# Performance work log

Measured on AMD Instinct MI355X. Metric: run time of the kernel, lower is better.

## Reference

```python
import jax, jax.numpy as jnp
import numpy as np

B, S, DM = 2, 2048, 1024
H, D = 16, 64  # multiheads, head_dim; H*D == DM
NEG = -1e9


def setup_inputs() -> dict:
    key = jax.random.key(0)
    ks = jax.random.split(key, 7)
    xavier = float(np.sqrt(6.0 / (DM + H * D)))
    return {
        "Q": jax.random.normal(ks[0], (B, S, DM), dtype=jnp.float32),
        "K": jax.random.normal(ks[1], (B, S, DM), dtype=jnp.float32),
        "V": jax.random.normal(ks[2], (B, S, DM), dtype=jnp.float32),
        "V_len": jax.random.randint(ks[3], (B,), 0, S),
        "WQ": jax.random.uniform(ks[4], (DM, H * D), dtype=jnp.float32, minval=-xavier, maxval=xavier),
        "WK": jax.random.uniform(ks[5], (DM, H * D), dtype=jnp.float32, minval=-xavier, maxval=xavier),
        "WV": jax.random.uniform(ks[6], (DM, H * D), dtype=jnp.float32, minval=-xavier, maxval=xavier),
    }


def reference(Q, K, V, V_len, WQ, WK, WV):
    b, s, _ = Q.shape
    # project and split heads: [B,S,DM] -> [B,H,S,D]
    q = (Q @ WQ).reshape(b, s, H, D).transpose(0, 2, 1, 3)
    k = (K @ WK).reshape(b, s, H, D).transpose(0, 2, 1, 3)
    v = (V @ WV).reshape(b, s, H, D).transpose(0, 2, 1, 3)
    scores = jnp.einsum("bhqd,bhkd->bhqk", q, k) / jnp.sqrt(jnp.float32(D))
    # key padding mask: valid keys are positions < V_len[b]
    valid = jnp.arange(s)[None, :] < V_len[:, None]          # [B,S]
    scores = jnp.where(valid[:, None, None, :], scores, NEG)  # [B,H,Sq,Sk]
    attn = jax.nn.softmax(scores, axis=-1)
    out = jnp.einsum("bhqk,bhkd->bhqd", attn, v)
    return out.transpose(0, 2, 1, 3).reshape(b, s, H * D)
```

## Files before the change

### kernel.cpp

```cpp
#include <hip/hip_runtime.h>
#include <hip/hip_bf16.h>

#define NBATCH 2
#define SEQ 2048
#define DMODEL 1024
#define NHEAD 16
#define HDIM 64
#define ROWS (NBATCH*SEQ)

typedef __attribute__((ext_vector_type(8))) short bf16x8;
typedef __attribute__((ext_vector_type(4))) float f32x4;
typedef __attribute__((ext_vector_type(16))) float f32x16;

#define MFMA16 __builtin_amdgcn_mfma_f32_16x16x32_bf16
#define MFMA32 __builtin_amdgcn_mfma_f32_32x32x16_bf16

#define QSCALE 0.1803368801111204f
#define DEFER_THR 11.541560327111708f

static __device__ __forceinline__ unsigned short f2bf(float f) {
    unsigned int u = __float_as_uint(f);
    u += 0x7fffu + ((u >> 16) & 1u);
    return (unsigned short)(u >> 16);
}

static __device__ __forceinline__ unsigned cvtpk(float lo, float hi) {
    unsigned r;
    asm("v_cvt_pk_bf16_f32 %0, %1, %2" : "=v"(r) : "v"(lo), "v"(hi));
    return r;
}

static __device__ __forceinline__ void gld16(const unsigned short* g, unsigned short* l) {
    __builtin_amdgcn_global_load_lds(
        (const __attribute__((address_space(1))) unsigned int*)g,
        (__attribute__((address_space(3))) unsigned int*)l,
        16, 0, 0);
}

__global__ __launch_bounds__(256) void cvt_kernel(const float* __restrict__ Q, const float* __restrict__ K,
                                                  const float* __restrict__ V, const int* __restrict__ vlenp,
                                                  unsigned short* __restrict__ dq, unsigned short* __restrict__ dk,
                                                  unsigned short* __restrict__ dv, int n8) {
    int i = blockIdx.x * 256 + threadIdx.x;
    if (i >= n8) return;
    const int z = blockIdx.z;
    if (z) {
        int row = i >> 7;
        int bb = row >> 11, s = row & 2047;
        int vl = vlenp[bb];
        int lim = ((vl + 31) >> 5) << 5;
        if (z == 1) { if (vl == 0 || s >= lim) return; }
        else        { if (vl != 0 && s >= lim) return; }
    }
    const float* src = z == 0 ? Q : (z == 1 ? K : V);
    unsigned short* dst = z == 0 ? dq : (z == 1 ? dk : dv);
    const float4* s4 = (const float4*)src;
    float4 a = s4[2 * i], b = s4[2 * i + 1];
    union { bf16x8 v; unsigned short u[8]; } o;
    o.u[0] = f2bf(a.x); o.u[1] = f2bf(a.y); o.u[2] = f2bf(a.z); o.u[3] = f2bf(a.w);
    o.u[4] = f2bf(b.x); o.u[5] = f2bf(b.y); o.u[6] = f2bf(b.z); o.u[7] = f2bf(b.w);
    *(bf16x8*)(dst + (size_t)i * 8) = o.v;
}

__global__ __launch_bounds__(256) void wtrans_kernel(const float* __restrict__ W0, const float* __restrict__ W1,
                                                     const float* __restrict__ W2,
                                                     unsigned short* __restrict__ T0, unsigned short* __restrict__ T1,
                                                     unsigned short* __restrict__ T2) {
    const float* W = blockIdx.z == 0 ? W0 : (blockIdx.z == 1 ? W1 : W2);
    unsigned short* T = blockIdx.z == 0 ? T0 : (blockIdx.z == 1 ? T1 : T2);
    __shared__ float tile[64][65];
    int rb = blockIdx.y * 64, cb = blockIdx.x * 64;
    int tid = threadIdx.x;
    #pragma unroll
    for (int rep = 0; rep < 16; ++rep) {
        int idx = rep * 256 + tid; int r = idx >> 6, c = idx & 63;
        tile[r][c] = W[(size_t)(rb + r) * DMODEL + cb + c];
    }
    __syncthreads();
    #pragma unroll
    for (int rep = 0; rep < 16; ++rep) {
        int idx = rep * 256 + tid; int r = idx >> 6, c = idx & 63;
        T[(size_t)(cb + r) * DMODEL + rb + c] = f2bf(tile[c][r]);
    }
}

__global__ __launch_bounds__(256) void proj_kernel(
        const unsigned short* __restrict__ Xq, const unsigned short* __restrict__ Xk,
        const unsigned short* __restrict__ Xv,
        const unsigned short* __restrict__ WTq, const unsigned short* __restrict__ WTk,
        const unsigned short* __restrict__ WTv, const int* __restrict__ vlenp,
        unsigned short* __restrict__ qp, unsigned short* __restrict__ kp,
        unsigned short* __restrict__ vtp) {
    const int mode = blockIdx.z;
    const int rowBase = blockIdx.y * 128;
    const int colBase = blockIdx.x * 128;

    if (mode >= 1) {
        const int bb = rowBase >> 11, sS = rowBase & 2047;
        const int vl = vlenp[bb];
        const int lim = ((vl + 31) >> 5) << 5;
        if (mode == 1) { if (vl == 0 || sS >= lim) return; }
        else           { if (vl != 0 && sS >= lim) return; }
    }

    const unsigned short* X  = mode == 0 ? Xq  : (mode == 1 ? Xk  : Xv);
    const unsigned short* WT = mode == 0 ? WTq : (mode == 1 ? WTk : WTv);

    __shared__ unsigned short As[128 * 64];
    __shared__ unsigned short Bs[128 * 64];

    const int tid = threadIdx.x, lane = tid & 63, w = tid >> 6;
    const int wr = w >> 1, wc = w & 1;

    const int Xwave = (mode < 2) ? wr : wc;
    const int Wwave = (mode < 2) ? wc : wr;

    const int rloc = lane >> 3;
    const int ssw  = ((lane & 7) * 8) ^ (rloc * 8);

    f32x4 acc[4][4];
    #pragma unroll
    for (int i = 0; i < 4; ++i)
        #pragma unroll
        for (int j = 0; j < 4; ++j) acc[i][j] = (f32x4){0.f, 0.f, 0.f, 0.f};

    for (int kt = 0; kt < DMODEL / 64; ++kt) {
        #pragma unroll
        for (int j = 0; j < 4; ++j) {
            int c = w * 4 + j;
            int r = c * 8 + rloc;
            gld16(X  + (size_t)(rowBase + r) * DMODEL + kt * 64 + ssw, &As[c * 512]);
            gld16(WT + (size_t)(colBase + r) * DMODEL + kt * 64 + ssw, &Bs[c * 512]);
        }
        __syncthreads();
        #pragma unroll
        for (int ks = 0; ks < 2; ++ks) {
            const int kbyte = ks * 64 + ((lane >> 4) * 16);
            bf16x8 xf[4], wf[4];
            #pragma unroll
            for (int i = 0; i < 4; ++i) {
                int xr = Xwave * 64 + i * 16 + (lane & 15);
                xf[i] = *(const bf16x8*)((const char*)As + xr * 128 + (kbyte ^ ((xr & 7) << 4)));
                int wrow = Wwave * 64 + i * 16 + (lane & 15);
                wf[i] = *(const bf16x8*)((const char*)Bs + wrow * 128 + (kbyte ^ ((wrow & 7) << 4)));
            }
            if (mode < 2) {
                #pragma unroll
                for (int i = 0; i < 4; ++i)
                    #pragma unroll
                    for (int j = 0; j < 4; ++j)
                        acc[i][j] = MFMA16(xf[i], wf[j], acc[i][j], 0, 0, 0);
            } else {
                #pragma unroll
                for (int i = 0; i < 4; ++i)
                    #pragma unroll
                    for (int j = 0; j < 4; ++j)
                        acc[i][j] = MFMA16(wf[i], xf[j], acc[i][j], 0, 0, 0);
            }
        }
        __syncthreads();
    }

    if (mode < 2) {
        unsigned short* outp = (mode == 0) ? qp : kp;
        const float sc = (mode == 0) ? QSCALE : 1.0f;
        #pragma unroll
        for (int i = 0; i < 4; ++i)
            #pragma unroll
            for (int j = 0; j < 4; ++j)
                #pragma unroll
                for (int r = 0; r < 4; ++r) {
                    int grow = rowBase + wr * 64 + i * 16 + (lane >> 4) * 4 + r;
                    int gcol = colBase + wc * 64 + j * 16 + (lane & 15);
                    int b = grow >> 11, s = grow & 2047, hh = gcol >> 6, d = gcol & 63;
                    outp[((size_t)(b * NHEAD + hh) * SEQ + s) * HDIM + d] = f2bf(acc[i][j][r] * sc);
                }
    } else {
        #pragma unroll
        for (int i = 0; i < 4; ++i)
            #pragma unroll
            for (int j = 0; j < 4; ++j)
                #pragma unroll
                for (int r = 0; r < 4; ++r) {
                    int gcol = colBase + wr * 64 + i * 16 + (lane >> 4) * 4 + r;
                    int grow = rowBase + wc * 64 + j * 16 + (lane & 15);
                    int b = grow >> 11, s = grow & 2047, hh = gcol >> 6, d = gcol & 63;
                    vtp[((size_t)(b * NHEAD + hh) * HDIM + d) * SEQ + s] = f2bf(acc[i][j][r]);
                }
    }
}

__global__ __launch_bounds__(256, 4) void attn_kernel(
        const unsigned short* __restrict__ qp, const unsigned short* __restrict__ kp,
        const unsigned short* __restrict__ vtp, const int* __restrict__ vlenp,
        float* __restrict__ out) {
    const int tid = threadIdx.x, lane = tid & 63, w = tid >> 6;
    const int hh = lane >> 5;
    const int ql = lane & 31;
    const int qsub = w >> 1, kpar = w & 1;
    const int qt = blockIdx.x, h = blockIdx.y, b = blockIdx.z;
    const int vlen = vlenp[b];
    const int nt = (vlen == 0) ? (SEQ / 32) : ((vlen + 31) >> 5);
    const int myn = (nt - kpar + 1) >> 1;

    __shared__ unsigned short Ks[4][2][32 * 64];
    __shared__ float mlb[4][2][32];

    const size_t headQ = (size_t)(b * NHEAD + h) * SEQ * HDIM;
    const size_t headV = (size_t)(b * NHEAD + h) * HDIM * SEQ;

    const int qrow = qt * 64 + qsub * 32 + ql;
    bf16x8 qf[4];
    #pragma unroll
    for (int ks = 0; ks < 4; ++ks)
        qf[ks] = *(const bf16x8*)(qp + headQ + (size_t)qrow * HDIM + ks * 16 + hh * 8);

    f32x16 o0, o1;
    #pragma unroll
    for (int r = 0; r < 16; ++r) { o0[r] = 0.f; o1[r] = 0.f; }
    float m_run = -1e30f, l_run = 0.f;

    const int rloc = lane >> 3;
    const int ssw  = ((lane & 7) * 8) ^ (rloc * 8);

    auto stage = [&](int kvB, int buf) {
        #pragma unroll
        for (int c = 0; c < 4; ++c)
            gld16(kp + headQ + (size_t)(kvB + c * 8 + rloc) * HDIM + ssw, &Ks[w][buf][c * 512]);
    };

    if (myn > 0) stage(kpar * 32, 0);

    for (int i = 0; i < myn; ++i) {
        const int kvBase = (kpar + 2 * i) * 32;
        const int cur = i & 1;
        asm volatile("s_waitcnt vmcnt(0)" ::: "memory");

        bf16x8 vf00 = *(const bf16x8*)(vtp + headV + (size_t)ql * SEQ + kvBase + hh * 8);
        bf16x8 vf01 = *(const bf16x8*)(vtp + headV + (size_t)(32 + ql) * SEQ + kvBase + hh * 8);
        bf16x8 vf10 = *(const bf16x8*)(vtp + headV + (size_t)ql * SEQ + kvBase + 16 + hh * 8);
        bf16x8 vf11 = *(const bf16x8*)(vtp + headV + (size_t)(32 + ql) * SEQ + kvBase + 16 + hh * 8);

        if (i + 1 < myn) stage(kvBase + 64, cur ^ 1);

        const char* Kb = (const char*)&Ks[w][cur][0];
        f32x16 s0;
        #pragma unroll
        for (int r = 0; r < 16; ++r) s0[r] = 0.f;
        __builtin_amdgcn_s_setprio(1);
        #pragma unroll
        for (int ks = 0; ks < 4; ++ks) {
            const int kb = (ks * 32 + hh * 16) ^ ((ql & 7) << 4);
            bf16x8 kf = *(const bf16x8*)(Kb + ql * 128 + kb);
            s0 = MFMA32(kf, qf[ks], s0, 0, 0, 0);
        }
        __builtin_amdgcn_s_setprio(0);

        if (kvBase + 32 > vlen) {
            #pragma unroll
            for (int r = 0; r < 16; ++r) {
                int kl = (r & 3) + 8 * (r >> 2) + 4 * hh;
                if (kvBase + kl >= vlen) s0[r] = -1e9f;
            }
        }

        float mx[8];
        #pragma unroll
        for (int t = 0; t < 8; ++t) mx[t] = fmaxf(s0[t], s0[t + 8]);
        #pragma unroll
        for (int st = 4; st > 0; st >>= 1)
            #pragma unroll
            for (int t = 0; t < st; ++t) mx[t] = fmaxf(mx[t], mx[t + st]);
        float tmax = fmaxf(mx[0], __shfl_xor(mx[0], 32));

        if (!__all(tmax <= m_run + DEFER_THR)) {
            const float mnew = fmaxf(m_run, tmax);
            const float al = __builtin_amdgcn_exp2f(m_run - mnew);
            l_run *= al;
            #pragma unroll
            for (int r = 0; r < 16; ++r) { o0[r] *= al; o1[r] *= al; }
            m_run = mnew;
        }

        #pragma unroll
        for (int r = 0; r < 16; ++r) s0[r] = __builtin_amdgcn_exp2f(s0[r] - m_run);
        float sm[8];
        #pragma unroll
        for (int t = 0; t < 8; ++t) sm[t] = s0[t] + s0[t + 8];
        #pragma unroll
        for (int st = 4; st > 0; st >>= 1)
            #pragma unroll
            for (int t = 0; t < st; ++t) sm[t] += sm[t + st];
        l_run += sm[0] + __shfl_xor(sm[0], 32);

        unsigned d0[8];
        #pragma unroll
        for (int t = 0; t < 8; ++t) d0[t] = cvtpk(s0[2 * t], s0[2 * t + 1]);

        __builtin_amdgcn_s_setprio(1);
#define PV_SLICE(KSL, VFA, VFB)                                                    \
        {                                                                          \
            unsigned a0 = d0[4 * (KSL)],     b0 = d0[4 * (KSL) + 2];               \
            unsigned a1 = d0[4 * (KSL) + 1], b1 = d0[4 * (KSL) + 3];               \
            asm("v_permlane32_swap_b32 %0, %1" : "+v"(a0), "+v"(b0));              \
            asm("v_permlane32_swap_b32 %0, %1" : "+v"(a1), "+v"(b1));              \
            union { unsigned u[4]; bf16x8 v; } pa;                                 \
            pa.u[0] = a0; pa.u[1] = a1; pa.u[2] = b0; pa.u[3] = b1;                \
            o0 = MFMA32(VFA, pa.v, o0, 0, 0, 0);                                   \
            o1 = MFMA32(VFB, pa.v, o1, 0, 0, 0);                                   \
        }
        PV_SLICE(0, vf00, vf01)
        PV_SLICE(1, vf10, vf11)
#undef PV_SLICE
        __builtin_amdgcn_s_setprio(0);
    }

    if (hh == 0) { mlb[w][0][ql] = m_run; mlb[w][1][ql] = l_run; }
    if (kpar == 1) {
        char* Ob = (char*)&Ks[w][0][0];
        #pragma unroll
        for (int g = 0; g < 4; ++g) {
            int ad = ql * 256 + ((32 * g + 16 * hh) ^ (16 * (ql & 7)));
            *(float4*)(Ob + ad)       = make_float4(o0[4*g], o0[4*g+1], o0[4*g+2], o0[4*g+3]);
            *(float4*)(Ob + ad + 128) = make_float4(o1[4*g], o1[4*g+1], o1[4*g+2], o1[4*g+3]);
        }
    }
    __syncthreads();
    if (kpar == 0) {
        const float mp = mlb[w + 1][0][ql], lp = mlb[w + 1][1][ql];
        const float M = fmaxf(m_run, mp);
        const float a0 = __builtin_amdgcn_exp2f(m_run - M);
        const float a1 = __builtin_amdgcn_exp2f(mp - M);
        const float linv = 1.0f / (l_run * a0 + lp * a1);
        const char* Pb = (const char*)&Ks[w + 1][0][0];
        float* orow = out + (size_t)(b * SEQ + qrow) * DMODEL + h * HDIM;
        #pragma unroll
        for (int g = 0; g < 4; ++g) {
            int ad = ql * 256 + ((32 * g + 16 * hh) ^ (16 * (ql & 7)));
            float4 p0 = *(const float4*)(Pb + ad);
            float4 p1 = *(const float4*)(Pb + ad + 128);
            *(float4*)(orow + 8 * g + 4 * hh) = make_float4(
                (o0[4*g]   * a0 + p0.x * a1) * linv, (o0[4*g+1] * a0 + p0.y * a1) * linv,
                (o0[4*g+2] * a0 + p0.z * a1) * linv, (o0[4*g+3] * a0 + p0.w * a1) * linv);
            *(float4*)(orow + 32 + 8 * g + 4 * hh) = make_float4(
                (o1[4*g]   * a0 + p1.x * a1) * linv, (o1[4*g+1] * a0 + p1.y * a1) * linv,
                (o1[4*g+2] * a0 + p1.z * a1) * linv, (o1[4*g+3] * a0 + p1.w * a1) * linv);
        }
    }
}

extern "C" void kernel_launch(void* const* d_in, const int* in_sizes, int n_in,
                              void* d_out, int out_size, void* d_ws, size_t ws_size,
                              hipStream_t stream) {
    const float* Q  = (const float*)d_in[0];
    const float* K  = (const float*)d_in[1];
    const float* V  = (const float*)d_in[2];
    const int* V_len = (const int*)d_in[3];
    const float* WQ = (const float*)d_in[4];
    const float* WK = (const float*)d_in[5];
    const float* WV = (const float*)d_in[6];
    float* out = (float*)d_out;

    char* ws = (char*)d_ws;
    const size_t MB = 1024 * 1024;
    unsigned short* Xq  = (unsigned short*)(ws + 0 * MB);
    unsigned short* Xk  = (unsigned short*)(ws + 8 * MB);
    unsigned short* Xv  = (unsigned short*)(ws + 16 * MB);
    unsigned short* WTq = (unsigned short*)(ws + 24 * MB);
    unsigned short* WTk = (unsigned short*)(ws + 26 * MB);
    unsigned short* WTv = (unsigned short*)(ws + 28 * MB);
    unsigned short* qpj = (unsigned short*)(ws + 30 * MB);
    unsigned short* kpj = (unsigned short*)(ws + 38 * MB);
    unsigned short* vtp = (unsigned short*)(ws + 46 * MB);

    const int n8 = ROWS * DMODEL / 8;
    cvt_kernel<<<dim3((n8 + 255) / 256, 1, 3), 256, 0, stream>>>(Q, K, V, V_len, Xq, Xk, Xv, n8);
    wtrans_kernel<<<dim3(16, 16, 3), 256, 0, stream>>>(WQ, WK, WV, WTq, WTk, WTv);
    proj_kernel<<<dim3(DMODEL / 128, ROWS / 128, 3), 256, 0, stream>>>(
        Xq, Xk, Xv, WTq, WTk, WTv, V_len, qpj, kpj, vtp);
    attn_kernel<<<dim3(SEQ / 64, NHEAD, NBATCH), 256, 0, stream>>>(qpj, kpj, vtp, V_len, out);
}
```

Before: 93.18 us.

## Share K and V tiles in LDS between wave pairs via cooperative staging

The two waves that handle the same key parity but different query sub-tiles now share one K tile and one V tile in LDS instead of each fetching its own. One wave stages the K tile and the other stages the V tile with async global-to-LDS loads, double-buffered. V fragments are read from swizzled LDS rather than loaded per wave straight from global memory. This halves global K/V traffic per block and makes the V reads more coalesced, at the cost of a block-wide __syncthreads each iteration and lockstep progress between waves, plus an extra barrier before the partial-output merge.

```diff
diff --git a/kernel.cpp b/kernel.cpp
--- a/kernel.cpp
+++ b/kernel.cpp
@@ -202,8 +202,10 @@
     const int vlen = vlenp[b];
     const int nt = (vlen == 0) ? (SEQ / 32) : ((vlen + 31) >> 5);
     const int myn = (nt - kpar + 1) >> 1;
-
-    __shared__ unsigned short Ks[4][2][32 * 64];
+    const int J = (nt + 1) >> 1;
+
+    __shared__ unsigned short Kd[2][2][2048];
+    __shared__ unsigned short Vd[2][2][2048];
     __shared__ float mlb[4][2][32];
 
     const size_t headQ = (size_t)(b * NHEAD + h) * SEQ * HDIM;
@@ -222,102 +224,116 @@
 
     const int rloc = lane >> 3;
     const int ssw  = ((lane & 7) * 8) ^ (rloc * 8);
-
-    auto stage = [&](int kvB, int buf) {
+    const int gn   = (lane & 7) ^ rloc;
+    const int koff = (gn & 3) * 8;
+    const int dhi  = (gn >> 2) * 32;
+
+    auto stageK = [&](int kvB, int buf) {
         #pragma unroll
         for (int c = 0; c < 4; ++c)
-            gld16(kp + headQ + (size_t)(kvB + c * 8 + rloc) * HDIM + ssw, &Ks[w][buf][c * 512]);
+            gld16(kp + headQ + (size_t)(kvB + c * 8 + rloc) * HDIM + ssw, &Kd[kpar][buf][c * 512]);
     };
-
-    if (myn > 0) stage(kpar * 32, 0);
-
-    for (int i = 0; i < myn; ++i) {
-        const int kvBase = (kpar + 2 * i) * 32;
-        const int cur = i & 1;
-        asm volatile("s_waitcnt vmcnt(0)" ::: "memory");
-
-        bf16x8 vf00 = *(const bf16x8*)(vtp + headV + (size_t)ql * SEQ + kvBase + hh * 8);
-        bf16x8 vf01 = *(const bf16x8*)(vtp + headV + (size_t)(32 + ql) * SEQ + kvBase + hh * 8);
-        bf16x8 vf10 = *(const bf16x8*)(vtp + headV + (size_t)ql * SEQ + kvBase + 16 + hh * 8);
-        bf16x8 vf11 = *(const bf16x8*)(vtp + headV + (size_t)(32 + ql) * SEQ + kvBase + 16 + hh * 8);
-
-        if (i + 1 < myn) stage(kvBase + 64, cur ^ 1);
-
-        const char* Kb = (const char*)&Ks[w][cur][0];
-        f32x16 s0;
-        #pragma unroll
-        for (int r = 0; r < 16; ++r) s0[r] = 0.f;
-        __builtin_amdgcn_s_setprio(1);
-        #pragma unroll
-        for (int ks = 0; ks < 4; ++ks) {
-            const int kb = (ks * 32 + hh * 16) ^ ((ql & 7) << 4);
-            bf16x8 kf = *(const bf16x8*)(Kb + ql * 128 + kb);
-            s0 = MFMA32(kf, qf[ks], s0, 0, 0, 0);
-        }
-        __builtin_amdgcn_s_setprio(0);
-
-        if (kvBase + 32 > vlen) {
-            #pragma unroll
-            for (int r = 0; r < 16; ++r) {
-                int kl = (r & 3) + 8 * (r >> 2) + 4 * hh;
-                if (kvBase + kl >= vlen) s0[r] = -1e9f;
-            }
-        }
-
-        float mx[8];
-        #pragma unroll
-        for (int t = 0; t < 8; ++t) mx[t] = fmaxf(s0[t], s0[t + 8]);
-        #pragma unroll
-        for (int st = 4; st > 0; st >>= 1)
-            #pragma unroll
-            for (int t = 0; t < st; ++t) mx[t] = fmaxf(mx[t], mx[t + st]);
-        float tmax = fmaxf(mx[0], __shfl_xor(mx[0], 32));
-
-        if (!__all(tmax <= m_run + DEFER_THR)) {
-            const float mnew = fmaxf(m_run, tmax);
-            const float al = __builtin_amdgcn_exp2f(m_run - mnew);
-            l_run *= al;
-            #pragma unroll
-            for (int r = 0; r < 16; ++r) { o0[r] *= al; o1[r] *= al; }
-            m_run = mnew;
-        }
-
-        #pragma unroll
-        for (int r = 0; r < 16; ++r) s0[r] = __builtin_amdgcn_exp2f(s0[r] - m_run);
-        float sm[8];
-        #pragma unroll
-        for (int t = 0; t < 8; ++t) sm[t] = s0[t] + s0[t + 8];
-        #pragma unroll
-        for (int st = 4; st > 0; st >>= 1)
-            #pragma unroll
-            for (int t = 0; t < st; ++t) sm[t] += sm[t + st];
-        l_run += sm[0] + __shfl_xor(sm[0], 32);
-
-        unsigned d0[8];
-        #pragma unroll
-        for (int t = 0; t < 8; ++t) d0[t] = cvtpk(s0[2 * t], s0[2 * t + 1]);
-
-        __builtin_amdgcn_s_setprio(1);
-#define PV_SLICE(KSL, VFA, VFB)                                                    \
-        {                                                                          \
-            unsigned a0 = d0[4 * (KSL)],     b0 = d0[4 * (KSL) + 2];               \
-            unsigned a1 = d0[4 * (KSL) + 1], b1 = d0[4 * (KSL) + 3];               \
-            asm("v_permlane32_swap_b32 %0, %1" : "+v"(a0), "+v"(b0));              \
-            asm("v_permlane32_swap_b32 %0, %1" : "+v"(a1), "+v"(b1));              \
-            union { unsigned u[4]; bf16x8 v; } pa;                                 \
-            pa.u[0] = a0; pa.u[1] = a1; pa.u[2] = b0; pa.u[3] = b1;                \
-            o0 = MFMA32(VFA, pa.v, o0, 0, 0, 0);                                   \
-            o1 = MFMA32(VFB, pa.v, o1, 0, 0, 0);                                   \
-        }
-        PV_SLICE(0, vf00, vf01)
-        PV_SLICE(1, vf10, vf11)
+    auto stageV = [&](int kvB, int buf) {
+        #pragma unroll
+        for (int c = 0; c < 4; ++c)
+            gld16(vtp + headV + (size_t)(c * 8 + rloc + dhi) * SEQ + kvB + koff, &Vd[kpar][buf][c * 512]);
+    };
+
+    if (myn > 0) { if (qsub == 0) stageK(kpar * 32, 0); else stageV(kpar * 32, 0); }
+
+    for (int j = 0; j < J; ++j) {
+        const int cur = j & 1;
+        __syncthreads();
+
+        if (j + 1 < myn) {
+            const int nb = (kpar + 2 * (j + 1)) * 32;
+            if (qsub == 0) stageK(nb, cur ^ 1); else stageV(nb, cur ^ 1);
+        }
+
+        if (j < myn) {
+            const int kvBase = (kpar + 2 * j) * 32;
+            const char* Kb = (const char*)&Kd[kpar][cur][0];
+            const char* Vb = (const char*)&Vd[kpar][cur][0];
+
+            f32x16 s0;
+            #pragma unroll
+            for (int r = 0; r < 16; ++r) s0[r] = 0.f;
+            __builtin_amdgcn_s_setprio(1);
+            #pragma unroll
+            for (int ks = 0; ks < 4; ++ks) {
+                const int kb = (ks * 32 + hh * 16) ^ ((ql & 7) << 4);
+                bf16x8 kf = *(const bf16x8*)(Kb + ql * 128 + kb);
+                s0 = MFMA32(kf, qf[ks], s0, 0, 0, 0);
+            }
+            __builtin_amdgcn_s_setprio(0);
+
+            if (kvBase + 32 > vlen) {
+                #pragma unroll
+                for (int r = 0; r < 16; ++r) {
+                    int kl = (r & 3) + 8 * (r >> 2) + 4 * hh;
+                    if (kvBase + kl >= vlen) s0[r] = -1e9f;
+                }
+            }
+
+            float mx[8];
+            #pragma unroll
+            for (int t = 0; t < 8; ++t) mx[t] = fmaxf(s0[t], s0[t + 8]);
+            #pragma unroll
+            for (int st = 4; st > 0; st >>= 1)
+                #pragma unroll
+                for (int t = 0; t < st; ++t) mx[t] = fmaxf(mx[t], mx[t + st]);
+            float tmax = fmaxf(mx[0], __shfl_xor(mx[0], 32));
+
+            if (!__all(tmax <= m_run + DEFER_THR)) {
+                const float mnew = fmaxf(m_run, tmax);
+                const float al = __builtin_amdgcn_exp2f(m_run - mnew);
+                l_run *= al;
+                #pragma unroll
+                for (int r = 0; r < 16; ++r) { o0[r] *= al; o1[r] *= al; }
+                m_run = mnew;
+            }
+
+            #pragma unroll
+            for (int r = 0; r < 16; ++r) s0[r] = __builtin_amdgcn_exp2f(s0[r] - m_run);
+            float sm[8];
+            #pragma unroll
+            for (int t = 0; t < 8; ++t) sm[t] = s0[t] + s0[t + 8];
+            #pragma unroll
+            for (int st = 4; st > 0; st >>= 1)
+                #pragma unroll
+                for (int t = 0; t < st; ++t) sm[t] += sm[t + st];
+            l_run += sm[0] + __shfl_xor(sm[0], 32);
+
+            unsigned d0[8];
+            #pragma unroll
+            for (int t = 0; t < 8; ++t) d0[t] = cvtpk(s0[2 * t], s0[2 * t + 1]);
+
+            __builtin_amdgcn_s_setprio(1);
+#define PV_SLICE(KSL)                                                              \
+            {                                                                      \
+                unsigned a0 = d0[4 * (KSL)],     b0 = d0[4 * (KSL) + 2];           \
+                unsigned a1 = d0[4 * (KSL) + 1], b1 = d0[4 * (KSL) + 3];           \
+                asm("v_permlane32_swap_b32 %0, %1" : "+v"(a0), "+v"(b0));          \
+                asm("v_permlane32_swap_b32 %0, %1" : "+v"(a1), "+v"(b1));          \
+                union { unsigned u[4]; bf16x8 v; } pa;                             \
+                pa.u[0] = a0; pa.u[1] = a1; pa.u[2] = b0; pa.u[3] = b1;            \
+                const int gA = 2 * (KSL) + hh;                                     \
+                bf16x8 vfA = *(const bf16x8*)(Vb + ql * 128 + ((gA ^ (ql & 7)) << 4));        \
+                bf16x8 vfB = *(const bf16x8*)(Vb + ql * 128 + (((4 + gA) ^ (ql & 7)) << 4));  \
+                o0 = MFMA32(vfA, pa.v, o0, 0, 0, 0);                               \
+                o1 = MFMA32(vfB, pa.v, o1, 0, 0, 0);                               \
+            }
+            PV_SLICE(0)
+            PV_SLICE(1)
 #undef PV_SLICE
-        __builtin_amdgcn_s_setprio(0);
+            __builtin_amdgcn_s_setprio(0);
+        }
     }
 
     if (hh == 0) { mlb[w][0][ql] = m_run; mlb[w][1][ql] = l_run; }
+    __syncthreads();
     if (kpar == 1) {
-        char* Ob = (char*)&Ks[w][0][0];
+        char* Ob = ((char*)Kd) + qsub * 8192;
         #pragma unroll
         for (int g = 0; g < 4; ++g) {
             int ad = ql * 256 + ((32 * g + 16 * hh) ^ (16 * (ql & 7)));
@@ -332,7 +348,7 @@
         const float a0 = __builtin_amdgcn_exp2f(m_run - M);
         const float a1 = __builtin_amdgcn_exp2f(mp - M);
         const float linv = 1.0f / (l_run * a0 + lp * a1);
-        const char* Pb = (const char*)&Ks[w + 1][0][0];
+        const char* Pb = ((const char*)Kd) + qsub * 8192;
         float* orow = out + (size_t)(b * SEQ + qrow) * DMODEL + h * HDIM;
         #pragma unroll
         for (int g = 0; g < 4; ++g) {
```

Measured after the change: 86.23 us. -7.5%, faster.
